# Performance work log

Measured on AMD Instinct MI355X. Metric: run time of the kernel, lower is better.

The kernel has to match this reference:

```python
import jax, jax.numpy as jnp
import numpy as np

B, N, FIN, H, D = 8, 2048, 64, 4, 32
ALPHA = 0.2  # LeakyReLU negative slope


def setup_inputs() -> dict:
    key = jax.random.key(0)
    k1, k2, k3, k4 = jax.random.split(key, 4)
    h = jax.random.normal(k1, (B, N, FIN), dtype=jnp.float32)
    adj = jax.random.randint(k2, (B, N, N), 0, 2).astype(jnp.int32)
    # ensure self-loops so every softmax row has at least one unmasked entry
    idx = jnp.arange(N)
    adj = adj.at[:, idx, idx].set(1)
    W = jax.random.normal(k3, (FIN, H * D), dtype=jnp.float32) * 0.1
    a = jax.random.normal(k4, (H, 2 * D), dtype=jnp.float32) * 0.1
    return {"h": h, "adj": adj, "W": W, "a": a}


def reference(h, adj, W, a):
    # h: (B,N,Fin), adj: (B,N,N) int, W: (Fin,H*D), a: (H,2D)
    Bn, Nn, _ = h.shape
    Hh, twoD = a.shape
    Dd = twoD // 2
    Wh = (h @ W).reshape(Bn, Nn, Hh, Dd).transpose(0, 2, 1, 3)  # (B,H,N,D)
    # e_ij = leakyrelu(Wh_i . a1 + Wh_j . a2) -- avoids O(N^2 * 2D) concat
    src = jnp.einsum('bhnd,hd->bhn', Wh, a[:, :Dd])  # (B,H,N)
    dst = jnp.einsum('bhnd,hd->bhn', Wh, a[:, Dd:])  # (B,H,N)
    e = jax.nn.leaky_relu(src[:, :, :, None] + dst[:, :, None, :], negative_slope=ALPHA)  # (B,H,N,N)
    e = jnp.where(adj[:, None, :, :] == 0, -jnp.inf, e)
    attn = jax.nn.softmax(e, axis=-1)  # (B,H,N,N)
    out = jnp.einsum('bhij,bhjd->bhid', attn, Wh)  # (B,H,N,D)
    return out.transpose(0, 2, 1, 3).reshape(Bn, Nn, Hh * Dd)
```

## Files before the change

kernel.cpp:

```cpp
#include <hip/hip_runtime.h>
#include <hip/hip_bf16.h>

typedef short short8 __attribute__((ext_vector_type(8)));
typedef float floatx4 __attribute__((ext_vector_type(4)));

#define B_   8
#define N_   2048
#define FIN_ 64
#define H_   4
#define D_   32
#define HD_  128
#define ALPHA_ 0.2f
#define LOG2E_ 1.4426950408889634f


__device__ __forceinline__ float fexp2(float x) {
#if __has_builtin(__builtin_amdgcn_exp2f)
    return __builtin_amdgcn_exp2f(x);
#else
    float r; asm("v_exp_f32 %0, %1" : "=v"(r) : "v"(x)); return r;
#endif
}

__device__ __forceinline__ unsigned pk2bf(float x, float y) {
    unsigned ux = __builtin_bit_cast(unsigned, x);
    ux = (ux + 0x7fffu + ((ux >> 16) & 1u)) >> 16;
    unsigned uy = __builtin_bit_cast(unsigned, y);
    uy = (uy + 0x7fffu + ((uy >> 16) & 1u)) >> 16;
    return ux | (uy << 16);
}

__device__ __forceinline__ unsigned pktrunc(float x, float y) {
    unsigned ux = __builtin_bit_cast(unsigned, x);
    unsigned uy = __builtin_bit_cast(unsigned, y);
#if __has_builtin(__builtin_amdgcn_perm)
    return __builtin_amdgcn_perm(uy, ux, 0x07060302u);
#else
    return (ux >> 16) | (uy & 0xffff0000u);
#endif
}

__global__ __launch_bounds__(256) void gat_prep2(
    const float* __restrict__ h, const float* __restrict__ W, const float* __restrict__ a,
    unsigned short* __restrict__ WhT, float* __restrict__ src, unsigned short* __restrict__ dstb)
{
    __shared__ float Ws[FIN_][HD_];
    __shared__ float hsT[FIN_][36];
    int bx = blockIdx.x;
    int b = bx >> 6;
    int n0 = (bx & 63) * 32;
    int tid = threadIdx.x;

    #pragma unroll
    for (int it = 0; it < 8; ++it) {
        int idx = it * 256 + tid;
        int k = idx >> 5, c4 = (idx & 31) << 2;
        *(float4*)&Ws[k][c4] = *(const float4*)&W[k * HD_ + c4];
    }
    #pragma unroll
    for (int it = 0; it < 8; ++it) {
        int idx = it * 256 + tid;
        int r = idx >> 6, k = idx & 63;
        hsT[k][r] = h[((size_t)b * N_ + n0 + r) * FIN_ + k];
    }
    __syncthreads();

    int c = tid & 127;
    int rq = tid >> 7;
    float acc[16];
    #pragma unroll
    for (int r = 0; r < 16; ++r) acc[r] = 0.f;
    for (int k = 0; k < FIN_; ++k) {
        float wv = Ws[k][c];
        float4 h0 = *(const float4*)&hsT[k][rq * 16];
        float4 h1 = *(const float4*)&hsT[k][rq * 16 + 4];
        float4 h2 = *(const float4*)&hsT[k][rq * 16 + 8];
        float4 h3 = *(const float4*)&hsT[k][rq * 16 + 12];
        acc[0]  += h0.x * wv; acc[1]  += h0.y * wv; acc[2]  += h0.z * wv; acc[3]  += h0.w * wv;
        acc[4]  += h1.x * wv; acc[5]  += h1.y * wv; acc[6]  += h1.z * wv; acc[7]  += h1.w * wv;
        acc[8]  += h2.x * wv; acc[9]  += h2.y * wv; acc[10] += h2.z * wv; acc[11] += h2.w * wv;
        acc[12] += h3.x * wv; acc[13] += h3.y * wv; acc[14] += h3.z * wv; acc[15] += h3.w * wv;
    }

    __attribute__((aligned(16))) unsigned pk[8];
    #pragma unroll
    for (int q = 0; q < 8; ++q) pk[q] = pk2bf(acc[2 * q], acc[2 * q + 1]);
    unsigned short* wrow = WhT + ((size_t)b * HD_ + c) * N_ + n0 + rq * 16;
    *(uint4*)wrow       = *(uint4*)&pk[0];
    *(uint4*)(wrow + 8) = *(uint4*)&pk[4];

    int hh = c >> 5, d = c & 31;
    float a1v = a[hh * 64 + d];
    float a2v = a[hh * 64 + 32 + d];
    #pragma unroll
    for (int r = 0; r < 16; ++r) {
        float s1 = acc[r] * a1v;
        float s2 = acc[r] * a2v;
        #pragma unroll
        for (int off = 16; off >= 1; off >>= 1) {
            s1 += __shfl_xor(s1, off, 32);
            s2 += __shfl_xor(s2, off, 32);
        }
        if (d == 0) {
            int n = n0 + rq * 16 + r;
            src[(b * H_ + hh) * N_ + n] = s1 * LOG2E_;
            unsigned u = __builtin_bit_cast(unsigned, s2 * LOG2E_);
            u = (u + 0x7fffu + ((u >> 16) & 1u)) >> 16;
            dstb[(b * H_ + hh) * N_ + n] = (unsigned short)u;
        }
    }
}

__global__ __launch_bounds__(256, 4) void gat_main7(
    const int* __restrict__ adj, const unsigned short* __restrict__ WhT,
    const float* __restrict__ src, const unsigned short* __restrict__ dstb,
    float* __restrict__ out)
{
    __shared__ unsigned short dsts[H_ * N_];
    __shared__ unsigned adjW[16][68];

    int bx = blockIdx.x;
    int b = bx >> 7;
    int i0 = (bx & 127) * 16;
    int tid = threadIdx.x;
    int wv = tid >> 6, l = tid & 63;

    #pragma unroll
    for (int it = 0; it < 4; ++it) {
        int idx = it * 256 + tid;
        *(uint4*)&dsts[idx * 8] = *(const uint4*)&dstb[(size_t)b * H_ * N_ + idx * 8];
    }

    const int* adjBase = adj + ((size_t)(b * N_ + i0 + wv * 4)) * N_ + l;

    int vals[32];
    #pragma unroll
    for (int rr = 0; rr < 4; ++rr)
        #pragma unroll
        for (int cc = 0; cc < 8; ++cc)
            vals[rr * 8 + cc] = adjBase[rr * N_ + cc * 64];

    int h = wv, g = l >> 4, m = l & 15;
    int g8 = g << 3;
    float src_r = src[(b * H_ + h) * N_ + i0 + m];
    const unsigned short* WhR0 = WhT + ((size_t)(b * H_ + h) * 32 + m) * N_;
    const unsigned short* WhR1 = WhR0 + (size_t)16 * N_;
    const unsigned short* dstH = &dsts[h * N_];

    short8 ones;
    #pragma unroll
    for (int q = 0; q < 8; ++q) ones[q] = (short)0x3F80;

    floatx4 acc0 = {0.f, 0.f, 0.f, 0.f};
    floatx4 acc1 = {0.f, 0.f, 0.f, 0.f};
    floatx4 acc2 = {0.f, 0.f, 0.f, 0.f};

    short8 bf0_c = *(const short8*)&WhR0[g8];
    short8 bf1_c = *(const short8*)&WhR1[g8];
    uint4 dv_c;

    for (int q = 0; q < 4; ++q) {
        #pragma unroll
        for (int rr = 0; rr < 4; ++rr)
            #pragma unroll
            for (int cc = 0; cc < 8; ++cc) {
                unsigned long long mk = __ballot(vals[rr * 8 + cc] != 0);
                if (l == 0) {
                    int c = q * 8 + cc;
                    adjW[wv * 4 + rr][2 * c]     = (unsigned)mk;
                    adjW[wv * 4 + rr][2 * c + 1] = (unsigned)(mk >> 32);
                }
            }
        __syncthreads();
        if (q == 0) dv_c = *(const uint4*)&dstH[g8];

        if (q < 3) {
            #pragma unroll
            for (int rr = 0; rr < 4; ++rr)
                #pragma unroll
                for (int cc = 0; cc < 8; ++cc)
                    vals[rr * 8 + cc] = adjBase[rr * N_ + (q + 1) * 512 + cc * 64];
        }

        for (int jj = 0; jj < 16; ++jj) {
            int it = q * 16 + jj;
            int j0n = ((it + 1) << 5) + g8;
            short8 bf0_n = *(const short8*)&WhR0[j0n];
            short8 bf1_n = *(const short8*)&WhR1[j0n];
            uint4  dv_n  = *(const uint4*)&dstH[(j0n < 2048) ? j0n : g8];

            unsigned sh = adjW[m][it] >> g8;
            const unsigned* du = (const unsigned*)&dv_c;
            unsigned pk[4];
            #pragma unroll
            for (int c2 = 0; c2 < 4; ++c2) {
                float dlo = __builtin_bit_cast(float, du[c2] << 16);
                float dhi = __builtin_bit_cast(float, du[c2] & 0xffff0000u);
                float e0 = src_r + dlo;
                float e1 = src_r + dhi;
                e0 = fmaxf(e0, ALPHA_ * e0);
                e1 = fmaxf(e1, ALPHA_ * e1);
                float m0 = (float)((sh >> (2 * c2)) & 1u);
                float m1 = (float)((sh >> (2 * c2 + 1)) & 1u);
                float x0 = fexp2(e0) * m0;
                float x1 = fexp2(e1) * m1;
                pk[c2] = pktrunc(x0, x1);
            }
            short8 af = __builtin_bit_cast(short8, *(uint4*)pk);
            acc0 = __builtin_amdgcn_mfma_f32_16x16x32_bf16(af, bf0_c, acc0, 0, 0, 0);
            acc1 = __builtin_amdgcn_mfma_f32_16x16x32_bf16(af, bf1_c, acc1, 0, 0, 0);
            acc2 = __builtin_amdgcn_mfma_f32_16x16x32_bf16(af, ones,  acc2, 0, 0, 0);
            bf0_c = bf0_n; bf1_c = bf1_n; dv_c = dv_n;
        }
    }

    #pragma unroll
    for (int r = 0; r < 4; ++r) {
        float inv = __builtin_amdgcn_rcpf(acc2[r]);
        size_t o = ((size_t)b * N_ + i0 + g * 4 + r) * HD_ + h * 32 + m;
        out[o]      = acc0[r] * inv;
        out[o + 16] = acc1[r] * inv;
    }
}

extern "C" void kernel_launch(void* const* d_in, const int* in_sizes, int n_in,
                              void* d_out, int out_size, void* d_ws, size_t ws_size,
                              hipStream_t stream) {
    const float* h   = (const float*)d_in[0];
    const int*   adj = (const int*)d_in[1];
    const float* W   = (const float*)d_in[2];
    const float* a   = (const float*)d_in[3];
    float* out = (float*)d_out;

    unsigned short* WhT  = (unsigned short*)d_ws;
    float*          src  = (float*)((char*)d_ws + 4u * 1024 * 1024);
    unsigned short* dstb = (unsigned short*)((char*)d_ws + 4u * 1024 * 1024 + 256u * 1024);

    gat_prep2<<<B_ * (N_ / 32), 256, 0, stream>>>(h, W, a, WhT, src, dstb);
    gat_main7<<<B_ * (N_ / 16), 256, 0, stream>>>(adj, WhT, src, dstb, out);
}
```

Baseline: 256.6 us.

## Split attention over key dimension into two halves with a separate combine kernel

The main GAT kernel now splits the j (neighbor) range into two halves handled by separate blocks, doubling the grid and halving per-block shared memory and register state so more blocks can be resident. Each half writes unnormalized partial outputs and row sums to workspace, and a new finalize kernel adds the two halves and normalizes. This trades an extra launch and extra global traffic (about 16 MB of partials) for more parallelism and occupancy. Because no running max is subtracted, the halves can be summed directly without rescaling.

```diff
diff --git a/kernel.cpp b/kernel.cpp
--- a/kernel.cpp
+++ b/kernel.cpp
@@ -10,6 +10,7 @@
 #define H_   4
 #define D_   32
 #define HD_  128
+#define JH_  1024
 #define ALPHA_ 0.2f
 #define LOG2E_ 1.4426950408889634f
 
@@ -111,41 +112,46 @@
     }
 }
 
-__global__ __launch_bounds__(256, 4) void gat_main7(
+__global__ __launch_bounds__(256, 8) void gat_main8(
     const int* __restrict__ adj, const unsigned short* __restrict__ WhT,
     const float* __restrict__ src, const unsigned short* __restrict__ dstb,
-    float* __restrict__ out)
+    float* __restrict__ pO, float* __restrict__ pW)
 {
-    __shared__ unsigned short dsts[H_ * N_];
-    __shared__ unsigned adjW[16][68];
+    __shared__ unsigned short dsts[H_ * JH_];
+    __shared__ unsigned adjW[16][36];
 
     int bx = blockIdx.x;
-    int b = bx >> 7;
-    int i0 = (bx & 127) * 16;
+    int b    = bx >> 8;
+    int rest = bx & 255;
+    int half = rest & 1;
+    int i0   = (rest >> 1) * 16;
+    int jb   = half * JH_;
     int tid = threadIdx.x;
     int wv = tid >> 6, l = tid & 63;
 
     #pragma unroll
-    for (int it = 0; it < 4; ++it) {
+    for (int it = 0; it < 2; ++it) {
         int idx = it * 256 + tid;
-        *(uint4*)&dsts[idx * 8] = *(const uint4*)&dstb[(size_t)b * H_ * N_ + idx * 8];
-    }
-
-    const int* adjBase = adj + ((size_t)(b * N_ + i0 + wv * 4)) * N_ + l;
-
-    int vals[32];
+        int hh = idx >> 7, off = (idx & 127) * 8;
+        *(uint4*)&dsts[hh * JH_ + off] =
+            *(const uint4*)&dstb[(size_t)(b * H_ + hh) * N_ + jb + off];
+    }
+
+    const int* adjBase = adj + ((size_t)(b * N_ + i0 + wv * 4)) * N_ + jb + l;
+
+    int vals[16];
     #pragma unroll
     for (int rr = 0; rr < 4; ++rr)
         #pragma unroll
-        for (int cc = 0; cc < 8; ++cc)
-            vals[rr * 8 + cc] = adjBase[rr * N_ + cc * 64];
+        for (int cc = 0; cc < 4; ++cc)
+            vals[rr * 4 + cc] = adjBase[rr * N_ + cc * 64];
 
     int h = wv, g = l >> 4, m = l & 15;
     int g8 = g << 3;
     float src_r = src[(b * H_ + h) * N_ + i0 + m];
-    const unsigned short* WhR0 = WhT + ((size_t)(b * H_ + h) * 32 + m) * N_;
+    const unsigned short* WhR0 = WhT + ((size_t)(b * H_ + h) * 32 + m) * N_ + jb;
     const unsigned short* WhR1 = WhR0 + (size_t)16 * N_;
-    const unsigned short* dstH = &dsts[h * N_];
+    const unsigned short* dstH = &dsts[h * JH_];
 
     short8 ones;
     #pragma unroll
@@ -163,10 +169,10 @@
         #pragma unroll
         for (int rr = 0; rr < 4; ++rr)
             #pragma unroll
-            for (int cc = 0; cc < 8; ++cc) {
-                unsigned long long mk = __ballot(vals[rr * 8 + cc] != 0);
+            for (int cc = 0; cc < 4; ++cc) {
+                unsigned long long mk = __ballot(vals[rr * 4 + cc] != 0);
                 if (l == 0) {
-                    int c = q * 8 + cc;
+                    int c = q * 4 + cc;
                     adjW[wv * 4 + rr][2 * c]     = (unsigned)mk;
                     adjW[wv * 4 + rr][2 * c + 1] = (unsigned)(mk >> 32);
                 }
@@ -178,16 +184,16 @@
             #pragma unroll
             for (int rr = 0; rr < 4; ++rr)
                 #pragma unroll
-                for (int cc = 0; cc < 8; ++cc)
-                    vals[rr * 8 + cc] = adjBase[rr * N_ + (q + 1) * 512 + cc * 64];
-        }
-
-        for (int jj = 0; jj < 16; ++jj) {
-            int it = q * 16 + jj;
+                for (int cc = 0; cc < 4; ++cc)
+                    vals[rr * 4 + cc] = adjBase[rr * N_ + (q + 1) * 256 + cc * 64];
+        }
+
+        for (int jj = 0; jj < 8; ++jj) {
+            int it = q * 8 + jj;
             int j0n = ((it + 1) << 5) + g8;
             short8 bf0_n = *(const short8*)&WhR0[j0n];
             short8 bf1_n = *(const short8*)&WhR1[j0n];
-            uint4  dv_n  = *(const uint4*)&dstH[(j0n < 2048) ? j0n : g8];
+            uint4  dv_n  = *(const uint4*)&dstH[(j0n < JH_) ? j0n : g8];
 
             unsigned sh = adjW[m][it] >> g8;
             const unsigned* du = (const unsigned*)&dv_c;
@@ -214,13 +220,39 @@
         }
     }
 
+    if (m == 0) {
+        #pragma unroll
+        for (int r = 0; r < 4; ++r)
+            pW[(((size_t)half * B_ + b) * H_ + h) * N_ + i0 + g * 4 + r] = acc2[r];
+    }
     #pragma unroll
     for (int r = 0; r < 4; ++r) {
-        float inv = __builtin_amdgcn_rcpf(acc2[r]);
-        size_t o = ((size_t)b * N_ + i0 + g * 4 + r) * HD_ + h * 32 + m;
-        out[o]      = acc0[r] * inv;
-        out[o + 16] = acc1[r] * inv;
-    }
+        size_t o = ((size_t)(half * B_ + b) * N_ + i0 + g * 4 + r) * HD_ + h * 32 + m;
+        pO[o]      = acc0[r];
+        pO[o + 16] = acc1[r];
+    }
+}
+
+__global__ __launch_bounds__(256) void gat_fin(
+    const float* __restrict__ pO, const float* __restrict__ pW, float* __restrict__ out)
+{
+    int gid = blockIdx.x * 256 + threadIdx.x;
+    int c4 = (gid & 31) << 2;
+    int i  = (gid >> 5) & (N_ - 1);
+    int b  = gid >> 16;
+    int hh = c4 >> 5;
+    float w0 = pW[((size_t)b * H_ + hh) * N_ + i];
+    float w1 = pW[(((size_t)B_ + b) * H_ + hh) * N_ + i];
+    float inv = 1.f / (w0 + w1);
+    size_t o = ((size_t)b * N_ + i) * HD_ + c4;
+    float4 v0 = *(const float4*)&pO[o];
+    float4 v1 = *(const float4*)&pO[(size_t)B_ * N_ * HD_ + o];
+    float4 r;
+    r.x = (v0.x + v1.x) * inv;
+    r.y = (v0.y + v1.y) * inv;
+    r.z = (v0.z + v1.z) * inv;
+    r.w = (v0.w + v1.w) * inv;
+    *(float4*)&out[o] = r;
 }
 
 extern "C" void kernel_launch(void* const* d_in, const int* in_sizes, int n_in,
@@ -235,7 +267,10 @@
     unsigned short* WhT  = (unsigned short*)d_ws;
     float*          src  = (float*)((char*)d_ws + 4u * 1024 * 1024);
     unsigned short* dstb = (unsigned short*)((char*)d_ws + 4u * 1024 * 1024 + 256u * 1024);
+    float*          pO   = (float*)((char*)d_ws + 8u * 1024 * 1024);
+    float*          pW   = (float*)((char*)d_ws + 24u * 1024 * 1024);
 
     gat_prep2<<<B_ * (N_ / 32), 256, 0, stream>>>(h, W, a, WhT, src, dstb);
-    gat_main7<<<B_ * (N_ / 16), 256, 0, stream>>>(adj, WhT, src, dstb, out);
-}
+    gat_main8<<<B_ * (N_ / 16) * 2, 256, 0, stream>>>(adj, WhT, src, dstb, pO, pW);
+    gat_fin<<<(B_ * N_ * HD_ / 4) / 256, 256, 0, stream>>>(pO, pW, out);
+}
```

New measurement: 276.2 us. 1.08x slower.
